# Kernel optimization log

Hardware: AMD Instinct MI355X
Metric: run time of the kernel (lower is better)

The kernel has to match this reference:

```python
import jax, jax.numpy as jnp
import numpy as np

N = [50000, 150000, 100000, 40000, 10000]  # cells per rank 0..4
C = 64       # channels (all ranks, in == out)
DEG = 8      # avg adjacency degree
INC = 4      # avg incidence nnz per higher-rank cell
PAIRS = [(0, 1), (1, 2), (2, 3), (3, 4)]


def _xavier(key, shape):
    s = float(np.sqrt(6.0 / (shape[0] + shape[1])))
    return jax.random.uniform(key, shape, jnp.float32, -s, s)


def setup_inputs() -> dict:
    key = jax.random.key(0)
    ks = iter(jax.random.split(key, 100))
    inp = {}
    for r in range(5):
        inp[f"x_{r}"] = jax.random.normal(next(ks), (N[r], C), jnp.float32)
        nnz = DEG * N[r]
        inp[f"a{r}_r"] = jax.random.randint(next(ks), (nnz,), 0, N[r], jnp.int32)
        inp[f"a{r}_c"] = jax.random.randint(next(ks), (nnz,), 0, N[r], jnp.int32)
        inp[f"a{r}_v"] = jax.random.uniform(next(ks), (nnz,), jnp.float32)
        inp[f"cci_{r}"] = jax.random.uniform(next(ks), (N[r], C), jnp.float32)
        inp[f"W_hbs_{r}"] = _xavier(next(ks), (C, C))
        inp[f"W_agg_{r}"] = _xavier(next(ks), (C, C))
    for a, b in PAIRS:
        nnz = INC * N[b]
        inp[f"i{a}{b}_t"] = jax.random.randint(next(ks), (nnz,), 0, N[a], jnp.int32)
        inp[f"i{a}{b}_s"] = jax.random.randint(next(ks), (nnz,), 0, N[b], jnp.int32)
        inp[f"i{a}{b}_v"] = jax.random.uniform(next(ks), (nnz,), jnp.float32)
        inp[f"W_s{a}{b}"] = _xavier(next(ks), (C, C))
        inp[f"W_t{a}{b}"] = _xavier(next(ks), (C, C))
    return inp


def _spmm(rows, cols, vals, x, n_out):
    # COO sparse matmul: out[i] = sum over entries e with rows[e]==i of vals[e]*x[cols[e]]
    return jax.ops.segment_sum(vals[:, None] * x[cols], rows, num_segments=n_out)


def _forward(x, av, cci, Wh, iv, Ws, Wt, Wg, ar, ac, it, isrc):
    relu = jax.nn.relu
    # HBS per rank: x_r_to_r = relu(cci_r * (A_r @ (x_r @ W_r)))
    same = [relu(cci[r] * _spmm(ar[r], ac[r], av[r], x[r] @ Wh[r], N[r])) for r in range(5)]
    down = {}  # message from rank b to rank a via incidence B_{a,b}
    up = {}    # message from rank a to rank b via B_{a,b}^T
    for k, (a, b) in enumerate(PAIRS):
        down[(b, a)] = relu(_spmm(it[k], isrc[k], iv[k], x[b] @ Ws[k], N[a]))
        up[(a, b)] = relu(_spmm(isrc[k], it[k], iv[k], x[a] @ Wt[k], N[b]))
    # RankAggregator: relu(sum(messages) @ W_agg)
    out0 = relu((same[0] + down[(1, 0)]) @ Wg[0])
    out1 = relu((up[(0, 1)] + same[1] + down[(2, 1)]) @ Wg[1])
    out2 = relu((up[(1, 2)] + same[2] + down[(3, 2)]) @ Wg[2])
    out3 = relu((up[(2, 3)] + same[3] + down[(4, 3)]) @ Wg[3])
    out4 = relu((up[(3, 4)] + same[4]) @ Wg[4])
    return (out0, out1, out2, out3, out4)


def reference(x_0, x_1, x_2, x_3, x_4,
              a0_r, a0_c, a0_v, a1_r, a1_c, a1_v, a2_r, a2_c, a2_v,
              a3_r, a3_c, a3_v, a4_r, a4_c, a4_v,
              cci_0, cci_1, cci_2, cci_3, cci_4,
              W_hbs_0, W_hbs_1, W_hbs_2, W_hbs_3, W_hbs_4,
              W_agg_0, W_agg_1, W_agg_2, W_agg_3, W_agg_4,
              i01_t, i01_s, i01_v, i12_t, i12_s, i12_v,
              i23_t, i23_s, i23_v, i34_t, i34_s, i34_v,
              W_s01, W_t01, W_s12, W_t12, W_s23, W_t23, W_s34, W_t34):
    return _forward([x_0, x_1, x_2, x_3, x_4],
                    [a0_v, a1_v, a2_v, a3_v, a4_v],
                    [cci_0, cci_1, cci_2, cci_3, cci_4],
                    [W_hbs_0, W_hbs_1, W_hbs_2, W_hbs_3, W_hbs_4],
                    [i01_v, i12_v, i23_v, i34_v],
                    [W_s01, W_s12, W_s23, W_s34],
                    [W_t01, W_t12, W_t23, W_t34],
                    [W_agg_0, W_agg_1, W_agg_2, W_agg_3, W_agg_4],
                    [a0_r, a1_r, a2_r, a3_r, a4_r],
                    [a0_c, a1_c, a2_c, a3_c, a4_c],
                    [i01_t, i12_t, i23_t, i34_t],
                    [i01_s, i12_s, i23_s, i34_s])
```

## Files before the change

kernel.cpp:

```cpp
#include <hip/hip_runtime.h>
#include <hip/hip_bf16.h>

__device__ __forceinline__ float bf2f(unsigned short u) {
    union { unsigned int i; float f; } v;
    v.i = ((unsigned int)u) << 16;
    return v.f;
}
__device__ __forceinline__ unsigned short f2bf(float f) {
    __hip_bfloat16 h = __float2bfloat16(f);
    return *reinterpret_cast<unsigned short*>(&h);
}

__global__ void probe_dtype(const unsigned short* __restrict__ x, int* flag) {
    if (blockIdx.x == 0 && threadIdx.x == 0) {
        int wild = 0;
        for (int i = 0; i < 512; ++i) {
            unsigned e = (x[i] >> 7) & 0xFF;
            if (e >= 0xC0) ++wild;
        }
        *flag = (wild > 0) ? 1 : 0;
    }
}

__global__ __launch_bounds__(256) void hist_rows(
    const int* __restrict__ rows, int* __restrict__ cnt, int nnz)
{
    int e = blockIdx.x * 256 + threadIdx.x;
    if (e < nnz) atomicAdd(&cnt[rows[e]], 1);
}

__global__ __launch_bounds__(256) void scan1(
    const int* __restrict__ cnt, int* __restrict__ rp, int* __restrict__ bsum, int n)
{
    __shared__ int s[256];
    const int b = blockIdx.x, t = threadIdx.x;
    const int base = b * 1024 + t * 4;
    int v[4]; int sum = 0;
#pragma unroll
    for (int j = 0; j < 4; ++j) { int i = base + j; v[j] = (i < n) ? cnt[i] : 0; sum += v[j]; }
    s[t] = sum; __syncthreads();
    for (int off = 1; off < 256; off <<= 1) {
        int xv = (t >= off) ? s[t - off] : 0;
        __syncthreads();
        s[t] += xv;
        __syncthreads();
    }
    int run = s[t] - sum;
#pragma unroll
    for (int j = 0; j < 4; ++j) { int i = base + j; if (i < n) rp[i] = run; run += v[j]; }
    if (t == 255) bsum[b] = s[255];
}

__global__ __launch_bounds__(256) void scan2(int* __restrict__ bsum, int nb)
{
    __shared__ int s[256];
    const int t = threadIdx.x;
    int v = (t < nb) ? bsum[t] : 0;
    s[t] = v; __syncthreads();
    for (int off = 1; off < 256; off <<= 1) {
        int xv = (t >= off) ? s[t - off] : 0;
        __syncthreads();
        s[t] += xv;
        __syncthreads();
    }
    if (t < nb) bsum[t] = s[t] - v;
}

__global__ __launch_bounds__(256) void scan3(
    int* __restrict__ rp, const int* __restrict__ bsum, int n, int nnz)
{
    int i = blockIdx.x * 256 + threadIdx.x;
    if (i < n) rp[i] += bsum[i >> 10];
    if (i == 0) rp[n] = nnz;
}

__global__ __launch_bounds__(256) void fill_edges(
    const int* __restrict__ rows, const int* __restrict__ cols,
    const void* __restrict__ vals, const int* __restrict__ flag,
    const int* __restrict__ rp, int* __restrict__ cur,
    uint2* __restrict__ edges, int nnz)
{
    int e = blockIdx.x * 256 + threadIdx.x;
    if (e >= nnz) return;
    int r = rows[e];
    int pos = rp[r] + atomicAdd(&cur[r], 1);
    float v = (*flag) ? ((const float*)vals)[e]
                      : bf2f(((const unsigned short*)vals)[e]);
    uint2 ed; ed.x = (unsigned)cols[e]; ed.y = __float_as_uint(v);
    edges[pos] = ed;
}

__global__ __launch_bounds__(256) void spmm_gemm(
    const int* __restrict__ rp, const uint2* __restrict__ edges,
    const void* __restrict__ x, const void* __restrict__ W,
    const void* __restrict__ cci, void* mout, const int* __restrict__ flag,
    int nrows, long long mbase, int mode)
{
    __shared__ float Ws[64][64];
    __shared__ float xs[64][65];
    const int tid = threadIdx.x;
    const int fl = *flag;

    if (fl) {
        const float* Wf = (const float*)W;
        for (int i = tid; i < 4096; i += 256) Ws[i >> 6][i & 63] = Wf[i];
    } else {
        const unsigned short* Wb = (const unsigned short*)W;
        for (int i = tid; i < 4096; i += 256) Ws[i >> 6][i & 63] = bf2f(Wb[i]);
    }

    const int row0 = blockIdx.x * 64;
    const int wv   = __builtin_amdgcn_readfirstlane(tid >> 6);
    const int lane = tid & 63;

    if (fl) {
        const float* xf = (const float*)x;
        for (int i = 0; i < 16; ++i) {
            int lr = wv * 16 + i;
            int row = row0 + lr;
            float a0 = 0.f, a1 = 0.f;
            if (row < nrows) {
                int e0 = rp[row], e1 = rp[row + 1];
                int e = e0;
                for (; e + 1 < e1; e += 2) {
                    uint2 d0 = edges[e], d1 = edges[e + 1];
                    a0 += __uint_as_float(d0.y) * xf[(size_t)d0.x * 64 + lane];
                    a1 += __uint_as_float(d1.y) * xf[(size_t)d1.x * 64 + lane];
                }
                if (e < e1) {
                    uint2 d0 = edges[e];
                    a0 += __uint_as_float(d0.y) * xf[(size_t)d0.x * 64 + lane];
                }
            }
            xs[lr][lane] = a0 + a1;
        }
    } else {
        const unsigned short* xb = (const unsigned short*)x;
        for (int i = 0; i < 16; ++i) {
            int lr = wv * 16 + i;
            int row = row0 + lr;
            float a0 = 0.f, a1 = 0.f;
            if (row < nrows) {
                int e0 = rp[row], e1 = rp[row + 1];
                int e = e0;
                for (; e + 1 < e1; e += 2) {
                    uint2 d0 = edges[e], d1 = edges[e + 1];
                    a0 += __uint_as_float(d0.y) * bf2f(xb[(size_t)d0.x * 64 + lane]);
                    a1 += __uint_as_float(d1.y) * bf2f(xb[(size_t)d1.x * 64 + lane]);
                }
                if (e < e1) {
                    uint2 d0 = edges[e];
                    a0 += __uint_as_float(d0.y) * bf2f(xb[(size_t)d0.x * 64 + lane]);
                }
            }
            xs[lr][lane] = a0 + a1;
        }
    }
    __syncthreads();

    const int tx = tid & 15, ty = tid >> 4;
    float a4[4][4];
#pragma unroll
    for (int a = 0; a < 4; ++a)
#pragma unroll
        for (int b = 0; b < 4; ++b) a4[a][b] = 0.f;

#pragma unroll 8
    for (int k = 0; k < 64; ++k) {
        float4 w4 = *reinterpret_cast<const float4*>(&Ws[k][tx << 2]);
#pragma unroll
        for (int rr = 0; rr < 4; ++rr) {
            float xv = xs[ty + 16 * rr][k];
            a4[rr][0] += xv * w4.x;
            a4[rr][1] += xv * w4.y;
            a4[rr][2] += xv * w4.z;
            a4[rr][3] += xv * w4.w;
        }
    }

#pragma unroll
    for (int rr = 0; rr < 4; ++rr) {
        int l = row0 + ty + 16 * rr;
        if (l >= nrows) continue;
        size_t co = (size_t)l * 64 + (tx << 2);
        size_t ob = (size_t)mbase + co;
        float t[4] = { a4[rr][0], a4[rr][1], a4[rr][2], a4[rr][3] };
        if (mode == 0) {
            float c4[4];
            if (fl) {
                float4 cv = *reinterpret_cast<const float4*>(&((const float*)cci)[co]);
                c4[0] = cv.x; c4[1] = cv.y; c4[2] = cv.z; c4[3] = cv.w;
            } else {
                ushort4 cv = *reinterpret_cast<const ushort4*>(&((const unsigned short*)cci)[co]);
                c4[0] = bf2f(cv.x); c4[1] = bf2f(cv.y); c4[2] = bf2f(cv.z); c4[3] = bf2f(cv.w);
            }
#pragma unroll
            for (int j = 0; j < 4; ++j) t[j] = fmaxf(t[j] * c4[j], 0.f);
            if (fl) {
                float4 o; o.x = t[0]; o.y = t[1]; o.z = t[2]; o.w = t[3];
                *reinterpret_cast<float4*>(&((float*)mout)[ob]) = o;
            } else {
                ushort4 o; o.x = f2bf(t[0]); o.y = f2bf(t[1]); o.z = f2bf(t[2]); o.w = f2bf(t[3]);
                *reinterpret_cast<ushort4*>(&((unsigned short*)mout)[ob]) = o;
            }
        } else {
            if (fl) {
                float* mp = (float*)mout;
                float4 ov = *reinterpret_cast<const float4*>(&mp[ob]);
                float4 o;
                o.x = ov.x + fmaxf(t[0], 0.f);
                o.y = ov.y + fmaxf(t[1], 0.f);
                o.z = ov.z + fmaxf(t[2], 0.f);
                o.w = ov.w + fmaxf(t[3], 0.f);
                *reinterpret_cast<float4*>(&mp[ob]) = o;
            } else {
                unsigned short* mp = (unsigned short*)mout;
                ushort4 ov = *reinterpret_cast<const ushort4*>(&mp[ob]);
                ushort4 o;
                o.x = f2bf(bf2f(ov.x) + fmaxf(t[0], 0.f));
                o.y = f2bf(bf2f(ov.y) + fmaxf(t[1], 0.f));
                o.z = f2bf(bf2f(ov.z) + fmaxf(t[2], 0.f));
                o.w = f2bf(bf2f(ov.w) + fmaxf(t[3], 0.f));
                *reinterpret_cast<ushort4*>(&mp[ob]) = o;
            }
        }
    }
}

__global__ __launch_bounds__(256) void scatter_x(
    const int* __restrict__ rows, const int* __restrict__ cols,
    const void* __restrict__ vals, const void* __restrict__ x,
    const int* __restrict__ flag,
    float* __restrict__ acc, int nnz, int r0, int r1)
{
    int e = blockIdx.x * 4 + threadIdx.y;
    if (e >= nnz) return;
    int r = rows[e];
    if (r < r0 || r >= r1) return;
    int c = threadIdx.x;
    int cc = cols[e];
    const int fl = *flag;
    float v, xv;
    if (fl) {
        v  = ((const float*)vals)[e];
        xv = ((const float*)x)[(size_t)cc * 64 + c];
    } else {
        v  = bf2f(((const unsigned short*)vals)[e]);
        xv = bf2f(((const unsigned short*)x)[(size_t)cc * 64 + c]);
    }
    atomicAdd(&acc[(size_t)(r - r0) * 64 + c], v * xv);
}

__global__ __launch_bounds__(256) void gemm_phase(
    const float* __restrict__ acc,
    const void* __restrict__ W,
    const void* __restrict__ cci,
    void* mout,
    const int* __restrict__ flag,
    int n_rows, long long grow0, long long mbase, int mode)
{
    __shared__ float Ws[64][64];
    __shared__ float xs[64][65];
    const int tid = threadIdx.x;
    const int tx = tid & 15, ty = tid >> 4;
    const int fl = *flag;

    if (fl) {
        const float* Wf = (const float*)W;
        for (int i = tid; i < 4096; i += 256) Ws[i >> 6][i & 63] = Wf[i];
    } else {
        const unsigned short* Wb = (const unsigned short*)W;
        for (int i = tid; i < 4096; i += 256) Ws[i >> 6][i & 63] = bf2f(Wb[i]);
    }
    const int lrow0 = blockIdx.x * 64;
    for (int i = tid; i < 4096; i += 256) {
        int r = i >> 6, c = i & 63;
        int l = lrow0 + r;
        xs[r][c] = (l < n_rows) ? acc[(size_t)l * 64 + c] : 0.f;
    }
    __syncthreads();

    float a4[4][4];
#pragma unroll
    for (int a = 0; a < 4; ++a)
#pragma unroll
        for (int b = 0; b < 4; ++b) a4[a][b] = 0.f;

#pragma unroll 8
    for (int k = 0; k < 64; ++k) {
        float4 w4 = *reinterpret_cast<const float4*>(&Ws[k][tx << 2]);
#pragma unroll
        for (int rr = 0; rr < 4; ++rr) {
            float xv = xs[ty + 16 * rr][k];
            a4[rr][0] += xv * w4.x;
            a4[rr][1] += xv * w4.y;
            a4[rr][2] += xv * w4.z;
            a4[rr][3] += xv * w4.w;
        }
    }

#pragma unroll
    for (int rr = 0; rr < 4; ++rr) {
        int l = lrow0 + ty + 16 * rr;
        if (l >= n_rows) continue;
        long long g = grow0 + l;
        size_t co = (size_t)g * 64 + (tx << 2);
        size_t ob = (size_t)mbase + co;
        float t[4] = { a4[rr][0], a4[rr][1], a4[rr][2], a4[rr][3] };
        if (mode == 0) {
            float c4[4];
            if (fl) {
                float4 cv = *reinterpret_cast<const float4*>(&((const float*)cci)[co]);
                c4[0] = cv.x; c4[1] = cv.y; c4[2] = cv.z; c4[3] = cv.w;
            } else {
                ushort4 cv = *reinterpret_cast<const ushort4*>(&((const unsigned short*)cci)[co]);
                c4[0] = bf2f(cv.x); c4[1] = bf2f(cv.y); c4[2] = bf2f(cv.z); c4[3] = bf2f(cv.w);
            }
#pragma unroll
            for (int j = 0; j < 4; ++j) t[j] = fmaxf(t[j] * c4[j], 0.f);
            if (fl) {
                float4 o; o.x = t[0]; o.y = t[1]; o.z = t[2]; o.w = t[3];
                *reinterpret_cast<float4*>(&((float*)mout)[ob]) = o;
            } else {
                ushort4 o; o.x = f2bf(t[0]); o.y = f2bf(t[1]); o.z = f2bf(t[2]); o.w = f2bf(t[3]);
                *reinterpret_cast<ushort4*>(&((unsigned short*)mout)[ob]) = o;
            }
        } else {
            if (fl) {
                float* mp = (float*)mout;
                float4 ov = *reinterpret_cast<const float4*>(&mp[ob]);
                float4 o;
                o.x = ov.x + fmaxf(t[0], 0.f);
                o.y = ov.y + fmaxf(t[1], 0.f);
                o.z = ov.z + fmaxf(t[2], 0.f);
                o.w = ov.w + fmaxf(t[3], 0.f);
                *reinterpret_cast<float4*>(&mp[ob]) = o;
            } else {
                unsigned short* mp = (unsigned short*)mout;
                ushort4 ov = *reinterpret_cast<const ushort4*>(&mp[ob]);
                ushort4 o;
                o.x = f2bf(bf2f(ov.x) + fmaxf(t[0], 0.f));
                o.y = f2bf(bf2f(ov.y) + fmaxf(t[1], 0.f));
                o.z = f2bf(bf2f(ov.z) + fmaxf(t[2], 0.f));
                o.w = f2bf(bf2f(ov.w) + fmaxf(t[3], 0.f));
                *reinterpret_cast<ushort4*>(&mp[ob]) = o;
            }
        }
    }
}

__global__ __launch_bounds__(256) void finalize(
    void* mout, const void* __restrict__ Wg, const int* __restrict__ flag,
    int N, long long mbase)
{
    __shared__ float Ws[64][64];
    __shared__ float ms[64][65];
    const int tid = threadIdx.x;
    const int tx = tid & 15, ty = tid >> 4;
    const int fl = *flag;

    if (fl) {
        const float* Wf = (const float*)Wg;
        for (int i = tid; i < 4096; i += 256) Ws[i >> 6][i & 63] = Wf[i];
    } else {
        const unsigned short* Wb = (const unsigned short*)Wg;
        for (int i = tid; i < 4096; i += 256) Ws[i >> 6][i & 63] = bf2f(Wb[i]);
    }
    const int row0 = blockIdx.x * 64;
    for (int i = tid; i < 4096; i += 256) {
        int r = i >> 6, c = i & 63;
        int g = row0 + r;
        float v = 0.f;
        if (g < N) {
            size_t o = (size_t)mbase + (size_t)g * 64 + c;
            v = fl ? ((const float*)mout)[o] : bf2f(((const unsigned short*)mout)[o]);
        }
        ms[r][c] = v;
    }
    __syncthreads();

    float a4[4][4];
#pragma unroll
    for (int a = 0; a < 4; ++a)
#pragma unroll
        for (int b = 0; b < 4; ++b) a4[a][b] = 0.f;

#pragma unroll 8
    for (int k = 0; k < 64; ++k) {
        float4 w4 = *reinterpret_cast<const float4*>(&Ws[k][tx << 2]);
#pragma unroll
        for (int rr = 0; rr < 4; ++rr) {
            float xv = ms[ty + 16 * rr][k];
            a4[rr][0] += xv * w4.x;
            a4[rr][1] += xv * w4.y;
            a4[rr][2] += xv * w4.z;
            a4[rr][3] += xv * w4.w;
        }
    }
#pragma unroll
    for (int rr = 0; rr < 4; ++rr) {
        int g = row0 + ty + 16 * rr;
        if (g >= N) continue;
        size_t ob = (size_t)mbase + (size_t)g * 64 + (tx << 2);
        if (fl) {
            float4 o;
            o.x = fmaxf(a4[rr][0], 0.f); o.y = fmaxf(a4[rr][1], 0.f);
            o.z = fmaxf(a4[rr][2], 0.f); o.w = fmaxf(a4[rr][3], 0.f);
            *reinterpret_cast<float4*>(&((float*)mout)[ob]) = o;
        } else {
            ushort4 o;
            o.x = f2bf(fmaxf(a4[rr][0], 0.f)); o.y = f2bf(fmaxf(a4[rr][1], 0.f));
            o.z = f2bf(fmaxf(a4[rr][2], 0.f)); o.w = f2bf(fmaxf(a4[rr][3], 0.f));
            *reinterpret_cast<ushort4*>(&((unsigned short*)mout)[ob]) = o;
        }
    }
}

extern "C" void kernel_launch(void* const* d_in, const int* in_sizes, int n_in,
                              void* d_out, int out_size, void* d_ws, size_t ws_size,
                              hipStream_t stream)
{
    static const int Ns[5] = {50000, 150000, 100000, 40000, 10000};

    const void *x[5], *av[5], *cci[5], *Whbs[5], *Wagg[5];
    const int *ar[5], *ac[5];
    int nnzA[5];
    for (int r = 0; r < 5; ++r) {
        x[r]    = d_in[r * 7 + 0];
        ar[r]   = (const int*)d_in[r * 7 + 1];
        ac[r]   = (const int*)d_in[r * 7 + 2];
        av[r]   = d_in[r * 7 + 3];
        cci[r]  = d_in[r * 7 + 4];
        Whbs[r] = d_in[r * 7 + 5];
        Wagg[r] = d_in[r * 7 + 6];
        nnzA[r] = in_sizes[r * 7 + 3];
    }
    const int *it[4], *is[4];
    const void *iv[4], *Wsp[4], *Wtp[4];
    int nnzI[4];
    for (int k = 0; k < 4; ++k) {
        it[k]  = (const int*)d_in[35 + k * 5 + 0];
        is[k]  = (const int*)d_in[35 + k * 5 + 1];
        iv[k]  = d_in[35 + k * 5 + 2];
        Wsp[k] = d_in[35 + k * 5 + 3];
        Wtp[k] = d_in[35 + k * 5 + 4];
        nnzI[k] = in_sizes[35 + k * 5 + 2];
    }

    char* ws = (char*)d_ws;
    size_t flag_off = (ws_size >= 4096) ? ((ws_size - 4) & ~(size_t)3) : 0;
    int* flag = (int*)(ws + flag_off);

    probe_dtype<<<1, 64, 0, stream>>>((const unsigned short*)x[0], flag);

    dim3 b256(256);
    dim3 sb(64, 4);
    long long base = 0;

    for (int r = 0; r < 5; ++r) {
        const int N = Ns[r];

        struct Ph { const int* rw; const int* cl; const void* vl; const void* xs;
                    const void* W; int nnz; int mode; };
        Ph ph[3]; int np = 0;
        ph[np++] = { ar[r], ac[r], av[r], x[r], Whbs[r], nnzA[r], 0 };
        if (r < 4) ph[np++] = { it[r], is[r], iv[r], x[r + 1], Wsp[r], nnzI[r], 1 };
        if (r > 0) ph[np++] = { is[r-1], it[r-1], iv[r-1], x[r - 1], Wtp[r-1], nnzI[r-1], 1 };

        for (int p = 0; p < np; ++p) {
            const int nnz = ph[p].nnz;
            size_t cntOff = 0;
            size_t rpOff  = ((size_t)N * 4 + 7) & ~(size_t)7;
            size_t bsOff  = rpOff + ((((size_t)N + 1) * 4 + 7) & ~(size_t)7);
            size_t edOff  = bsOff + 4096;
            size_t need   = edOff + (size_t)nnz * 8;

            if (need + 64 <= flag_off) {
                int*   cnt = (int*)(ws + cntOff);
                int*   rp  = (int*)(ws + rpOff);
                int*   bs  = (int*)(ws + bsOff);
                uint2* ed  = (uint2*)(ws + edOff);
                const int nb = (N + 1023) / 1024;

                hipMemsetAsync(cnt, 0, (size_t)N * 4, stream);
                hist_rows<<<(nnz + 255) / 256, b256, 0, stream>>>(ph[p].rw, cnt, nnz);
                scan1<<<nb, b256, 0, stream>>>(cnt, rp, bs, N);
                scan2<<<1, b256, 0, stream>>>(bs, nb);
                scan3<<<(N + 255) / 256, b256, 0, stream>>>(rp, bs, N, nnz);
                hipMemsetAsync(cnt, 0, (size_t)N * 4, stream);
                fill_edges<<<(nnz + 255) / 256, b256, 0, stream>>>(
                    ph[p].rw, ph[p].cl, ph[p].vl, flag, rp, cnt, ed, nnz);
                spmm_gemm<<<(N + 63) / 64, b256, 0, stream>>>(
                    rp, ed, ph[p].xs, ph[p].W, cci[r], d_out, flag,
                    N, base, ph[p].mode);
            } else {
                long long budget = (long long)((flag_off - 256) / 256);
                budget &= ~63LL;
                if (budget < 64) budget = 64;
                float* acc = (float*)ws;
                for (long long r0 = 0; r0 < N; r0 += budget) {
                    int rc = (int)((N - r0 < budget) ? (N - r0) : budget);
                    hipMemsetAsync(acc, 0, (size_t)rc * 256, stream);
                    scatter_x<<<(nnz + 3) / 4, sb, 0, stream>>>(
                        ph[p].rw, ph[p].cl, ph[p].vl, ph[p].xs, flag,
                        acc, nnz, (int)r0, (int)(r0 + rc));
                    gemm_phase<<<(rc + 63) / 64, b256, 0, stream>>>(
                        acc, ph[p].W, cci[r], d_out, flag,
                        rc, r0, base, ph[p].mode);
                }
            }
        }
        finalize<<<(N + 63) / 64, b256, 0, stream>>>(d_out, Wagg[r], flag, N, base);
        base += (long long)N * 64;
    }
}
```

Measured before the change: 1.804 ms.

## Fuse per-rank message phases and aggregation into one kernel with batched CSR build

Batches the CSR construction for all of a rank's message phases into single launches indexed by blockIdx.y. The scan is simplified: the second pass recomputes each block prefix by a reduction, and the separate cursor array is replaced by atomic increments on the row pointer. A new rank_fused kernel gathers, multiplies and accumulates every phase in registers, then applies the aggregation GEMM directly, so partial messages no longer round-trip through global memory and finalize is skipped. The gather loop is unrolled by 8 with row pointers shared across lanes by shuffle, and shared memory uses an XOR swizzle instead of padding. The cost is more workspace for the simultaneous CSR buffers and higher register pressure in the fused kernel.

Result: faster. 1.555 ms (-13.8%).

```diff
diff --git a/kernel.cpp b/kernel.cpp
--- a/kernel.cpp
+++ b/kernel.cpp
@@ -10,6 +10,7 @@
     __hip_bfloat16 h = __float2bfloat16(f);
     return *reinterpret_cast<unsigned short*>(&h);
 }
+__device__ __forceinline__ int xc(int r, int c) { return c ^ ((r & 3) << 3); }
 
 __global__ void probe_dtype(const unsigned short* __restrict__ x, int* flag) {
     if (blockIdx.x == 0 && threadIdx.x == 0) {
@@ -22,84 +23,268 @@
     }
 }
 
-__global__ __launch_bounds__(256) void hist_rows(
-    const int* __restrict__ rows, int* __restrict__ cnt, int nnz)
+struct Seg {
+    const int*  rows;
+    const int*  cols;
+    const void* vals;
+    int*  cnt;
+    int*  rp;
+    int*  bsum;
+    uint2* ed;
+    int nnz;
+    int n;
+};
+struct Seg3 { Seg s[3]; };
+
+__global__ __launch_bounds__(256) void hist_all(Seg3 B) {
+    Seg S = B.s[blockIdx.y];
+    int e = blockIdx.x * 256 + threadIdx.x;
+    if (e < S.nnz) atomicAdd(&S.cnt[S.rows[e]], 1);
+}
+
+__global__ __launch_bounds__(256) void scan1_all(Seg3 B) {
+    Seg S = B.s[blockIdx.y];
+    __shared__ int sm[256];
+    const int t = threadIdx.x;
+    const int base = blockIdx.x * 1024 + t * 4;
+    int v[4]; int sum = 0;
+#pragma unroll
+    for (int j = 0; j < 4; ++j) { int i = base + j; v[j] = (i < S.n) ? S.cnt[i] : 0; sum += v[j]; }
+    sm[t] = sum; __syncthreads();
+    for (int off = 1; off < 256; off <<= 1) {
+        int xv = (t >= off) ? sm[t - off] : 0;
+        __syncthreads();
+        sm[t] += xv;
+        __syncthreads();
+    }
+    int run = sm[t] - sum;
+#pragma unroll
+    for (int j = 0; j < 4; ++j) { int i = base + j; if (i < S.n) S.rp[i] = run; run += v[j]; }
+    if (t == 255) S.bsum[blockIdx.x] = sm[255];
+}
+
+__global__ __launch_bounds__(256) void scan2_all(Seg3 B) {
+    Seg S = B.s[blockIdx.y];
+    __shared__ int red[256];
+    const int t = threadIdx.x;
+    const int g0 = blockIdx.x >> 2;
+    int v = (t < g0) ? S.bsum[t] : 0;
+    red[t] = v; __syncthreads();
+    for (int o = 128; o; o >>= 1) { if (t < o) red[t] += red[t + o]; __syncthreads(); }
+    int i = blockIdx.x * 256 + t;
+    if (i < S.n) S.rp[i] += red[0];
+}
+
+__global__ __launch_bounds__(256) void fill_all(Seg3 B, const int* __restrict__ flag) {
+    Seg S = B.s[blockIdx.y];
+    int e = blockIdx.x * 256 + threadIdx.x;
+    if (e >= S.nnz) return;
+    int r = S.rows[e];
+    int pos = atomicAdd(&S.rp[r], 1);
+    float v = (*flag) ? ((const float*)S.vals)[e]
+                      : bf2f(((const unsigned short*)S.vals)[e]);
+    uint2 ed; ed.x = (unsigned)S.cols[e]; ed.y = __float_as_uint(v);
+    S.ed[pos] = ed;
+}
+
+template<int FL>
+__device__ __forceinline__ void gather16(
+    const int* __restrict__ rp, const uint2* __restrict__ ed,
+    const void* __restrict__ x, float xsh[64][64],
+    int row0, int nrows, int wv, int lane)
 {
-    int e = blockIdx.x * 256 + threadIdx.x;
-    if (e < nnz) atomicAdd(&cnt[rows[e]], 1);
-}
-
-__global__ __launch_bounds__(256) void scan1(
-    const int* __restrict__ cnt, int* __restrict__ rp, int* __restrict__ bsum, int n)
+    const int rbase = row0 + wv * 16;
+    int rv = 0;
+    {
+        int t = rbase - 1 + lane;
+        if (lane <= 16 && t >= 0 && t < nrows) rv = rp[t];
+    }
+    for (int i = 0; i < 16; ++i) {
+        int row = rbase + i;
+        int e0 = __shfl(rv, i, 64);
+        int e1 = __shfl(rv, i + 1, 64);
+        float acc = 0.f;
+        if (row < nrows) {
+            for (int e = e0; e < e1; e += 8) {
+                uint2 d[8];
+#pragma unroll
+                for (int j = 0; j < 8; ++j) {
+                    int idx = e + j;
+                    idx = (idx < e1) ? idx : (e1 - 1);
+                    d[j] = ed[idx];
+                }
+                float xv[8];
+#pragma unroll
+                for (int j = 0; j < 8; ++j) {
+                    size_t off = (size_t)d[j].x * 64 + lane;
+                    xv[j] = FL ? ((const float*)x)[off]
+                               : bf2f(((const unsigned short*)x)[off]);
+                }
+#pragma unroll
+                for (int j = 0; j < 8; ++j) {
+                    float v = (e + j < e1) ? __uint_as_float(d[j].y) : 0.f;
+                    acc = fmaf(v, xv[j], acc);
+                }
+            }
+        }
+        xsh[wv * 16 + i][xc(wv * 16 + i, lane)] = acc;
+    }
+}
+
+struct RankArgs {
+    const int*   rp[3];
+    const uint2* ed[3];
+    const void*  xsrc[3];
+    const void*  W[3];
+    const void*  cci;
+    const void*  Wg;
+    long long    mbase;
+    int          nrows;
+    int          nph;
+};
+
+__global__ __launch_bounds__(256, 4) void rank_fused(
+    RankArgs A, void* __restrict__ dout, const int* __restrict__ flag)
 {
-    __shared__ int s[256];
-    const int b = blockIdx.x, t = threadIdx.x;
-    const int base = b * 1024 + t * 4;
-    int v[4]; int sum = 0;
-#pragma unroll
-    for (int j = 0; j < 4; ++j) { int i = base + j; v[j] = (i < n) ? cnt[i] : 0; sum += v[j]; }
-    s[t] = sum; __syncthreads();
-    for (int off = 1; off < 256; off <<= 1) {
-        int xv = (t >= off) ? s[t - off] : 0;
+    __shared__ float Ws[64][64];
+    __shared__ float xsh[64][64];
+    const int tid = threadIdx.x;
+    const int fl = *flag;
+    const int row0 = blockIdx.x * 64;
+    const int wv   = __builtin_amdgcn_readfirstlane(tid >> 6);
+    const int lane = tid & 63;
+    const int tx = tid & 15, ty = tid >> 4;
+
+    float C[4][4];
+#pragma unroll
+    for (int a = 0; a < 4; ++a)
+#pragma unroll
+        for (int b = 0; b < 4; ++b) C[a][b] = 0.f;
+
+    for (int p = 0; p < A.nph; ++p) {
         __syncthreads();
-        s[t] += xv;
+        if (fl) {
+            const float* Wf = (const float*)A.W[p];
+            for (int i = tid; i < 4096; i += 256) Ws[i >> 6][i & 63] = Wf[i];
+        } else {
+            const unsigned short* Wb = (const unsigned short*)A.W[p];
+            for (int i = tid; i < 4096; i += 256) Ws[i >> 6][i & 63] = bf2f(Wb[i]);
+        }
+        if (fl) gather16<1>(A.rp[p], A.ed[p], A.xsrc[p], xsh, row0, A.nrows, wv, lane);
+        else    gather16<0>(A.rp[p], A.ed[p], A.xsrc[p], xsh, row0, A.nrows, wv, lane);
         __syncthreads();
-    }
-    int run = s[t] - sum;
-#pragma unroll
-    for (int j = 0; j < 4; ++j) { int i = base + j; if (i < n) rp[i] = run; run += v[j]; }
-    if (t == 255) bsum[b] = s[255];
-}
-
-__global__ __launch_bounds__(256) void scan2(int* __restrict__ bsum, int nb)
-{
-    __shared__ int s[256];
-    const int t = threadIdx.x;
-    int v = (t < nb) ? bsum[t] : 0;
-    s[t] = v; __syncthreads();
-    for (int off = 1; off < 256; off <<= 1) {
-        int xv = (t >= off) ? s[t - off] : 0;
-        __syncthreads();
-        s[t] += xv;
-        __syncthreads();
-    }
-    if (t < nb) bsum[t] = s[t] - v;
-}
-
-__global__ __launch_bounds__(256) void scan3(
-    int* __restrict__ rp, const int* __restrict__ bsum, int n, int nnz)
-{
-    int i = blockIdx.x * 256 + threadIdx.x;
-    if (i < n) rp[i] += bsum[i >> 10];
-    if (i == 0) rp[n] = nnz;
-}
-
-__global__ __launch_bounds__(256) void fill_edges(
-    const int* __restrict__ rows, const int* __restrict__ cols,
-    const void* __restrict__ vals, const int* __restrict__ flag,
-    const int* __restrict__ rp, int* __restrict__ cur,
-    uint2* __restrict__ edges, int nnz)
-{
-    int e = blockIdx.x * 256 + threadIdx.x;
-    if (e >= nnz) return;
-    int r = rows[e];
-    int pos = rp[r] + atomicAdd(&cur[r], 1);
-    float v = (*flag) ? ((const float*)vals)[e]
-                      : bf2f(((const unsigned short*)vals)[e]);
-    uint2 ed; ed.x = (unsigned)cols[e]; ed.y = __float_as_uint(v);
-    edges[pos] = ed;
-}
-
-__global__ __launch_bounds__(256) void spmm_gemm(
+
+        float a4[4][4];
+#pragma unroll
+        for (int a = 0; a < 4; ++a)
+#pragma unroll
+            for (int b = 0; b < 4; ++b) a4[a][b] = 0.f;
+
+#pragma unroll 8
+        for (int k = 0; k < 64; ++k) {
+            float4 w4 = *reinterpret_cast<const float4*>(&Ws[k][tx << 2]);
+#pragma unroll
+            for (int rr = 0; rr < 4; ++rr) {
+                int r = ty + 16 * rr;
+                float xv = xsh[r][xc(r, k)];
+                a4[rr][0] += xv * w4.x;
+                a4[rr][1] += xv * w4.y;
+                a4[rr][2] += xv * w4.z;
+                a4[rr][3] += xv * w4.w;
+            }
+        }
+
+        if (p == 0) {
+#pragma unroll
+            for (int rr = 0; rr < 4; ++rr) {
+                int l = row0 + ty + 16 * rr;
+                if (l >= A.nrows) continue;
+                size_t co = (size_t)l * 64 + (tx << 2);
+                float c4[4];
+                if (fl) {
+                    float4 cv = *reinterpret_cast<const float4*>(&((const float*)A.cci)[co]);
+                    c4[0] = cv.x; c4[1] = cv.y; c4[2] = cv.z; c4[3] = cv.w;
+                } else {
+                    ushort4 cv = *reinterpret_cast<const ushort4*>(&((const unsigned short*)A.cci)[co]);
+                    c4[0] = bf2f(cv.x); c4[1] = bf2f(cv.y); c4[2] = bf2f(cv.z); c4[3] = bf2f(cv.w);
+                }
+#pragma unroll
+                for (int j = 0; j < 4; ++j) C[rr][j] += fmaxf(a4[rr][j] * c4[j], 0.f);
+            }
+        } else {
+#pragma unroll
+            for (int rr = 0; rr < 4; ++rr)
+#pragma unroll
+                for (int j = 0; j < 4; ++j) C[rr][j] += fmaxf(a4[rr][j], 0.f);
+        }
+    }
+
+    __syncthreads();
+#pragma unroll
+    for (int rr = 0; rr < 4; ++rr) {
+        int r = ty + 16 * rr;
+#pragma unroll
+        for (int j = 0; j < 4; ++j) xsh[r][xc(r, (tx << 2) + j)] = C[rr][j];
+    }
+    if (fl) {
+        const float* Wf = (const float*)A.Wg;
+        for (int i = tid; i < 4096; i += 256) Ws[i >> 6][i & 63] = Wf[i];
+    } else {
+        const unsigned short* Wb = (const unsigned short*)A.Wg;
+        for (int i = tid; i < 4096; i += 256) Ws[i >> 6][i & 63] = bf2f(Wb[i]);
+    }
+    __syncthreads();
+
+    float a4[4][4];
+#pragma unroll
+    for (int a = 0; a < 4; ++a)
+#pragma unroll
+        for (int b = 0; b < 4; ++b) a4[a][b] = 0.f;
+#pragma unroll 8
+    for (int k = 0; k < 64; ++k) {
+        float4 w4 = *reinterpret_cast<const float4*>(&Ws[k][tx << 2]);
+#pragma unroll
+        for (int rr = 0; rr < 4; ++rr) {
+            int r = ty + 16 * rr;
+            float xv = xsh[r][xc(r, k)];
+            a4[rr][0] += xv * w4.x;
+            a4[rr][1] += xv * w4.y;
+            a4[rr][2] += xv * w4.z;
+            a4[rr][3] += xv * w4.w;
+        }
+    }
+#pragma unroll
+    for (int rr = 0; rr < 4; ++rr) {
+        int l = row0 + ty + 16 * rr;
+        if (l >= A.nrows) continue;
+        size_t ob = (size_t)A.mbase + (size_t)l * 64 + (tx << 2);
+        if (fl) {
+            float4 o;
+            o.x = fmaxf(a4[rr][0], 0.f); o.y = fmaxf(a4[rr][1], 0.f);
+            o.z = fmaxf(a4[rr][2], 0.f); o.w = fmaxf(a4[rr][3], 0.f);
+            *reinterpret_cast<float4*>(&((float*)dout)[ob]) = o;
+        } else {
+            ushort4 o;
+            o.x = f2bf(fmaxf(a4[rr][0], 0.f)); o.y = f2bf(fmaxf(a4[rr][1], 0.f));
+            o.z = f2bf(fmaxf(a4[rr][2], 0.f)); o.w = f2bf(fmaxf(a4[rr][3], 0.f));
+            *reinterpret_cast<ushort4*>(&((unsigned short*)dout)[ob]) = o;
+        }
+    }
+}
+
+__global__ __launch_bounds__(256, 4) void spmm_gemm(
     const int* __restrict__ rp, const uint2* __restrict__ edges,
     const void* __restrict__ x, const void* __restrict__ W,
     const void* __restrict__ cci, void* mout, const int* __restrict__ flag,
     int nrows, long long mbase, int mode)
 {
     __shared__ float Ws[64][64];
-    __shared__ float xs[64][65];
+    __shared__ float xsh[64][64];
     const int tid = threadIdx.x;
     const int fl = *flag;
+    const int row0 = blockIdx.x * 64;
+    const int wv   = __builtin_amdgcn_readfirstlane(tid >> 6);
+    const int lane = tid & 63;
 
     if (fl) {
         const float* Wf = (const float*)W;
@@ -108,54 +293,8 @@
         const unsigned short* Wb = (const unsigned short*)W;
         for (int i = tid; i < 4096; i += 256) Ws[i >> 6][i & 63] = bf2f(Wb[i]);
     }
-
-    const int row0 = blockIdx.x * 64;
-    const int wv   = __builtin_amdgcn_readfirstlane(tid >> 6);
-    const int lane = tid & 63;
-
-    if (fl) {
-        const float* xf = (const float*)x;
-        for (int i = 0; i < 16; ++i) {
-            int lr = wv * 16 + i;
-            int row = row0 + lr;
-            float a0 = 0.f, a1 = 0.f;
-            if (row < nrows) {
-                int e0 = rp[row], e1 = rp[row + 1];
-                int e = e0;
-                for (; e + 1 < e1; e += 2) {
-                    uint2 d0 = edges[e], d1 = edges[e + 1];
-                    a0 += __uint_as_float(d0.y) * xf[(size_t)d0.x * 64 + lane];
-                    a1 += __uint_as_float(d1.y) * xf[(size_t)d1.x * 64 + lane];
-                }
-                if (e < e1) {
-                    uint2 d0 = edges[e];
-                    a0 += __uint_as_float(d0.y) * xf[(size_t)d0.x * 64 + lane];
-                }
-            }
-            xs[lr][lane] = a0 + a1;
-        }
-    } else {
-        const unsigned short* xb = (const unsigned short*)x;
-        for (int i = 0; i < 16; ++i) {
-            int lr = wv * 16 + i;
-            int row = row0 + lr;
-            float a0 = 0.f, a1 = 0.f;
-            if (row < nrows) {
-                int e0 = rp[row], e1 = rp[row + 1];
-                int e = e0;
-                for (; e + 1 < e1; e += 2) {
-                    uint2 d0 = edges[e], d1 = edges[e + 1];
-                    a0 += __uint_as_float(d0.y) * bf2f(xb[(size_t)d0.x * 64 + lane]);
-                    a1 += __uint_as_float(d1.y) * bf2f(xb[(size_t)d1.x * 64 + lane]);
-                }
-                if (e < e1) {
-                    uint2 d0 = edges[e];
-                    a0 += __uint_as_float(d0.y) * bf2f(xb[(size_t)d0.x * 64 + lane]);
-                }
-            }
-            xs[lr][lane] = a0 + a1;
-        }
-    }
+    if (fl) gather16<1>(rp, edges, x, xsh, row0, nrows, wv, lane);
+    else    gather16<0>(rp, edges, x, xsh, row0, nrows, wv, lane);
     __syncthreads();
 
     const int tx = tid & 15, ty = tid >> 4;
@@ -170,7 +309,8 @@
         float4 w4 = *reinterpret_cast<const float4*>(&Ws[k][tx << 2]);
 #pragma unroll
         for (int rr = 0; rr < 4; ++rr) {
-            float xv = xs[ty + 16 * rr][k];
+            int r = ty + 16 * rr;
+            float xv = xsh[r][xc(r, k)];
             a4[rr][0] += xv * w4.x;
             a4[rr][1] += xv * w4.y;
             a4[rr][2] += xv * w4.z;
@@ -223,6 +363,73 @@
                 o.w = f2bf(bf2f(ov.w) + fmaxf(t[3], 0.f));
                 *reinterpret_cast<ushort4*>(&mp[ob]) = o;
             }
+        }
+    }
+}
+
+__global__ __launch_bounds__(256) void finalize(
+    void* mout, const void* __restrict__ Wg, const int* __restrict__ flag,
+    int N, long long mbase)
+{
+    __shared__ float Ws[64][64];
+    __shared__ float ms[64][65];
+    const int tid = threadIdx.x;
+    const int tx = tid & 15, ty = tid >> 4;
+    const int fl = *flag;
+
+    if (fl) {
+        const float* Wf = (const float*)Wg;
+        for (int i = tid; i < 4096; i += 256) Ws[i >> 6][i & 63] = Wf[i];
+    } else {
+        const unsigned short* Wb = (const unsigned short*)Wg;
+        for (int i = tid; i < 4096; i += 256) Ws[i >> 6][i & 63] = bf2f(Wb[i]);
+    }
+    const int row0 = blockIdx.x * 64;
+    for (int i = tid; i < 4096; i += 256) {
+        int r = i >> 6, c = i & 63;
+        int g = row0 + r;
+        float v = 0.f;
+        if (g < N) {
+            size_t o = (size_t)mbase + (size_t)g * 64 + c;
+            v = fl ? ((const float*)mout)[o] : bf2f(((const unsigned short*)mout)[o]);
+        }
+        ms[r][c] = v;
+    }
+    __syncthreads();
+
+    float a4[4][4];
+#pragma unroll
+    for (int a = 0; a < 4; ++a)
+#pragma unroll
+        for (int b = 0; b < 4; ++b) a4[a][b] = 0.f;
+
+#pragma unroll 8
+    for (int k = 0; k < 64; ++k) {
+        float4 w4 = *reinterpret_cast<const float4*>(&Ws[k][tx << 2]);
+#pragma unroll
+        for (int rr = 0; rr < 4; ++rr) {
+            float xv = ms[ty + 16 * rr][k];
+            a4[rr][0] += xv * w4.x;
+            a4[rr][1] += xv * w4.y;
+            a4[rr][2] += xv * w4.z;
+            a4[rr][3] += xv * w4.w;
+        }
+    }
+#pragma unroll
+    for (int rr = 0; rr < 4; ++rr) {
+        int g = row0 + ty + 16 * rr;
+        if (g >= N) continue;
+        size_t ob = (size_t)mbase + (size_t)g * 64 + (tx << 2);
+        if (fl) {
+            float4 o;
+            o.x = fmaxf(a4[rr][0], 0.f); o.y = fmaxf(a4[rr][1], 0.f);
+            o.z = fmaxf(a4[rr][2], 0.f); o.w = fmaxf(a4[rr][3], 0.f);
+            *reinterpret_cast<float4*>(&((float*)mout)[ob]) = o;
+        } else {
+            ushort4 o;
+            o.x = f2bf(fmaxf(a4[rr][0], 0.f)); o.y = f2bf(fmaxf(a4[rr][1], 0.f));
+            o.z = f2bf(fmaxf(a4[rr][2], 0.f)); o.w = f2bf(fmaxf(a4[rr][3], 0.f));
+            *reinterpret_cast<ushort4*>(&((unsigned short*)mout)[ob]) = o;
         }
     }
 }
@@ -349,73 +556,6 @@
     }
 }
 
-__global__ __launch_bounds__(256) void finalize(
-    void* mout, const void* __restrict__ Wg, const int* __restrict__ flag,
-    int N, long long mbase)
-{
-    __shared__ float Ws[64][64];
-    __shared__ float ms[64][65];
-    const int tid = threadIdx.x;
-    const int tx = tid & 15, ty = tid >> 4;
-    const int fl = *flag;
-
-    if (fl) {
-        const float* Wf = (const float*)Wg;
-        for (int i = tid; i < 4096; i += 256) Ws[i >> 6][i & 63] = Wf[i];
-    } else {
-        const unsigned short* Wb = (const unsigned short*)Wg;
-        for (int i = tid; i < 4096; i += 256) Ws[i >> 6][i & 63] = bf2f(Wb[i]);
-    }
-    const int row0 = blockIdx.x * 64;
-    for (int i = tid; i < 4096; i += 256) {
-        int r = i >> 6, c = i & 63;
-        int g = row0 + r;
-        float v = 0.f;
-        if (g < N) {
-            size_t o = (size_t)mbase + (size_t)g * 64 + c;
-            v = fl ? ((const float*)mout)[o] : bf2f(((const unsigned short*)mout)[o]);
-        }
-        ms[r][c] = v;
-    }
-    __syncthreads();
-
-    float a4[4][4];
-#pragma unroll
-    for (int a = 0; a < 4; ++a)
-#pragma unroll
-        for (int b = 0; b < 4; ++b) a4[a][b] = 0.f;
-
-#pragma unroll 8
-    for (int k = 0; k < 64; ++k) {
-        float4 w4 = *reinterpret_cast<const float4*>(&Ws[k][tx << 2]);
-#pragma unroll
-        for (int rr = 0; rr < 4; ++rr) {
-            float xv = ms[ty + 16 * rr][k];
-            a4[rr][0] += xv * w4.x;
-            a4[rr][1] += xv * w4.y;
-            a4[rr][2] += xv * w4.z;
-            a4[rr][3] += xv * w4.w;
-        }
-    }
-#pragma unroll
-    for (int rr = 0; rr < 4; ++rr) {
-        int g = row0 + ty + 16 * rr;
-        if (g >= N) continue;
-        size_t ob = (size_t)mbase + (size_t)g * 64 + (tx << 2);
-        if (fl) {
-            float4 o;
-            o.x = fmaxf(a4[rr][0], 0.f); o.y = fmaxf(a4[rr][1], 0.f);
-            o.z = fmaxf(a4[rr][2], 0.f); o.w = fmaxf(a4[rr][3], 0.f);
-            *reinterpret_cast<float4*>(&((float*)mout)[ob]) = o;
-        } else {
-            ushort4 o;
-            o.x = f2bf(fmaxf(a4[rr][0], 0.f)); o.y = f2bf(fmaxf(a4[rr][1], 0.f));
-            o.z = f2bf(fmaxf(a4[rr][2], 0.f)); o.w = f2bf(fmaxf(a4[rr][3], 0.f));
-            *reinterpret_cast<ushort4*>(&((unsigned short*)mout)[ob]) = o;
-        }
-    }
-}
-
 extern "C" void kernel_launch(void* const* d_in, const int* in_sizes, int n_in,
                               void* d_out, int out_size, void* d_ws, size_t ws_size,
                               hipStream_t stream)
@@ -453,64 +593,103 @@
 
     probe_dtype<<<1, 64, 0, stream>>>((const unsigned short*)x[0], flag);
 
+    auto al16 = [](size_t v) { return (v + 15) & ~(size_t)15; };
     dim3 b256(256);
-    dim3 sb(64, 4);
     long long base = 0;
 
     for (int r = 0; r < 5; ++r) {
         const int N = Ns[r];
 
         struct Ph { const int* rw; const int* cl; const void* vl; const void* xs;
-                    const void* W; int nnz; int mode; };
+                    const void* W; int nnz; };
         Ph ph[3]; int np = 0;
-        ph[np++] = { ar[r], ac[r], av[r], x[r], Whbs[r], nnzA[r], 0 };
-        if (r < 4) ph[np++] = { it[r], is[r], iv[r], x[r + 1], Wsp[r], nnzI[r], 1 };
-        if (r > 0) ph[np++] = { is[r-1], it[r-1], iv[r-1], x[r - 1], Wtp[r-1], nnzI[r-1], 1 };
-
-        for (int p = 0; p < np; ++p) {
-            const int nnz = ph[p].nnz;
-            size_t cntOff = 0;
-            size_t rpOff  = ((size_t)N * 4 + 7) & ~(size_t)7;
-            size_t bsOff  = rpOff + ((((size_t)N + 1) * 4 + 7) & ~(size_t)7);
-            size_t edOff  = bsOff + 4096;
-            size_t need   = edOff + (size_t)nnz * 8;
-
-            if (need + 64 <= flag_off) {
-                int*   cnt = (int*)(ws + cntOff);
-                int*   rp  = (int*)(ws + rpOff);
-                int*   bs  = (int*)(ws + bsOff);
-                uint2* ed  = (uint2*)(ws + edOff);
-                const int nb = (N + 1023) / 1024;
-
-                hipMemsetAsync(cnt, 0, (size_t)N * 4, stream);
-                hist_rows<<<(nnz + 255) / 256, b256, 0, stream>>>(ph[p].rw, cnt, nnz);
-                scan1<<<nb, b256, 0, stream>>>(cnt, rp, bs, N);
-                scan2<<<1, b256, 0, stream>>>(bs, nb);
-                scan3<<<(N + 255) / 256, b256, 0, stream>>>(rp, bs, N, nnz);
-                hipMemsetAsync(cnt, 0, (size_t)N * 4, stream);
-                fill_edges<<<(nnz + 255) / 256, b256, 0, stream>>>(
-                    ph[p].rw, ph[p].cl, ph[p].vl, flag, rp, cnt, ed, nnz);
-                spmm_gemm<<<(N + 63) / 64, b256, 0, stream>>>(
-                    rp, ed, ph[p].xs, ph[p].W, cci[r], d_out, flag,
-                    N, base, ph[p].mode);
-            } else {
-                long long budget = (long long)((flag_off - 256) / 256);
-                budget &= ~63LL;
-                if (budget < 64) budget = 64;
-                float* acc = (float*)ws;
-                for (long long r0 = 0; r0 < N; r0 += budget) {
-                    int rc = (int)((N - r0 < budget) ? (N - r0) : budget);
-                    hipMemsetAsync(acc, 0, (size_t)rc * 256, stream);
-                    scatter_x<<<(nnz + 3) / 4, sb, 0, stream>>>(
-                        ph[p].rw, ph[p].cl, ph[p].vl, ph[p].xs, flag,
-                        acc, nnz, (int)r0, (int)(r0 + rc));
-                    gemm_phase<<<(rc + 63) / 64, b256, 0, stream>>>(
-                        acc, ph[p].W, cci[r], d_out, flag,
-                        rc, r0, base, ph[p].mode);
+        ph[np++] = { ar[r], ac[r], av[r], x[r], Whbs[r], nnzA[r] };
+        if (r < 4) ph[np++] = { it[r], is[r], iv[r], x[r + 1], Wsp[r], nnzI[r] };
+        if (r > 0) ph[np++] = { is[r-1], it[r-1], iv[r-1], x[r - 1], Wtp[r-1], nnzI[r-1] };
+
+        size_t cntOff = 0;
+        size_t rpOff  = al16((size_t)np * N * 4);
+        size_t bsOff  = rpOff + al16((size_t)np * N * 4);
+        size_t edOff  = al16(bsOff + (size_t)np * 256 * 4);
+        size_t edSz = 0;
+        for (int p = 0; p < np; ++p) edSz += al16((size_t)ph[p].nnz * 8);
+        size_t need = edOff + edSz;
+
+        if (need + 64 <= flag_off) {
+            Seg3 B{};
+            size_t ep = edOff;
+            int maxnnz = 0;
+            for (int p = 0; p < np; ++p) {
+                B.s[p].rows = ph[p].rw;  B.s[p].cols = ph[p].cl;  B.s[p].vals = ph[p].vl;
+                B.s[p].cnt  = (int*)(ws + cntOff) + (size_t)p * N;
+                B.s[p].rp   = (int*)(ws + rpOff)  + (size_t)p * N;
+                B.s[p].bsum = (int*)(ws + bsOff)  + (size_t)p * 256;
+                B.s[p].ed   = (uint2*)(ws + ep);
+                B.s[p].nnz  = ph[p].nnz;
+                B.s[p].n    = N;
+                ep += al16((size_t)ph[p].nnz * 8);
+                if (ph[p].nnz > maxnnz) maxnnz = ph[p].nnz;
+            }
+            hipMemsetAsync(ws + cntOff, 0, (size_t)np * N * 4, stream);
+            hist_all <<<dim3((maxnnz + 255) / 256, np), b256, 0, stream>>>(B);
+            scan1_all<<<dim3((N + 1023) / 1024, np), b256, 0, stream>>>(B);
+            scan2_all<<<dim3((N + 255) / 256, np), b256, 0, stream>>>(B);
+            fill_all <<<dim3((maxnnz + 255) / 256, np), b256, 0, stream>>>(B, flag);
+
+            RankArgs A{};
+            for (int p = 0; p < np; ++p) {
+                A.rp[p]   = B.s[p].rp;
+                A.ed[p]   = B.s[p].ed;
+                A.xsrc[p] = ph[p].xs;
+                A.W[p]    = ph[p].W;
+            }
+            A.cci = cci[r]; A.Wg = Wagg[r];
+            A.mbase = base; A.nrows = N; A.nph = np;
+            rank_fused<<<(N + 63) / 64, b256, 0, stream>>>(A, d_out, flag);
+        } else {
+            for (int p = 0; p < np; ++p) {
+                const int nnz = ph[p].nnz;
+                size_t cOff = 0;
+                size_t rOff = al16((size_t)N * 4);
+                size_t bOff = rOff + al16((size_t)N * 4);
+                size_t eOff = al16(bOff + 1024);
+                size_t need3 = eOff + (size_t)nnz * 8;
+                if (need3 + 64 <= flag_off) {
+                    Seg3 B{};
+                    B.s[0].rows = ph[p].rw; B.s[0].cols = ph[p].cl; B.s[0].vals = ph[p].vl;
+                    B.s[0].cnt  = (int*)(ws + cOff);
+                    B.s[0].rp   = (int*)(ws + rOff);
+                    B.s[0].bsum = (int*)(ws + bOff);
+                    B.s[0].ed   = (uint2*)(ws + eOff);
+                    B.s[0].nnz  = nnz; B.s[0].n = N;
+                    hipMemsetAsync(ws + cOff, 0, (size_t)N * 4, stream);
+                    hist_all <<<dim3((nnz + 255) / 256, 1), b256, 0, stream>>>(B);
+                    scan1_all<<<dim3((N + 1023) / 1024, 1), b256, 0, stream>>>(B);
+                    scan2_all<<<dim3((N + 255) / 256, 1), b256, 0, stream>>>(B);
+                    fill_all <<<dim3((nnz + 255) / 256, 1), b256, 0, stream>>>(B, flag);
+                    spmm_gemm<<<(N + 63) / 64, b256, 0, stream>>>(
+                        B.s[0].rp, B.s[0].ed, ph[p].xs, ph[p].W, cci[r], d_out, flag,
+                        N, base, (p == 0) ? 0 : 1);
+                } else {
+                    long long budget = (flag_off > 256) ? (long long)((flag_off - 256) / 256) : 64;
+                    budget &= ~63LL;
+                    if (budget < 64) budget = 64;
+                    float* acc = (float*)ws;
+                    dim3 sb(64, 4);
+                    for (long long r0 = 0; r0 < N; r0 += budget) {
+                        int rc = (int)((N - r0 < budget) ? (N - r0) : budget);
+                        hipMemsetAsync(acc, 0, (size_t)rc * 256, stream);
+                        scatter_x<<<(nnz + 3) / 4, sb, 0, stream>>>(
+                            ph[p].rw, ph[p].cl, ph[p].vl, ph[p].xs, flag,
+                            acc, nnz, (int)r0, (int)(r0 + rc));
+                        gemm_phase<<<(rc + 63) / 64, b256, 0, stream>>>(
+                            acc, ph[p].W, cci[r], d_out, flag,
+                            rc, r0, base, (p == 0) ? 0 : 1);
+                    }
                 }
             }
-        }
-        finalize<<<(N + 63) / 64, b256, 0, stream>>>(d_out, Wagg[r], flag, N, base);
+            finalize<<<(N + 63) / 64, b256, 0, stream>>>(d_out, Wagg[r], flag, N, base);
+        }
         base += (long long)N * 64;
     }
 }
```
